# Kernel optimization log

Measured on AMD Instinct MI355X. Metric: run time of the kernel, lower is better.

Reference implementation:

```python
import jax, jax.numpy as jnp
import numpy as np

N_NODES = 50000


def _gcn_conv(x, W, b, src, dst, n_nodes):
    """PyG GCNConv: add self-loops, D^-1/2 (A+I) D^-1/2 X W + b."""
    loop = jnp.arange(n_nodes, dtype=src.dtype)
    src_f = jnp.concatenate([src, loop])  # [E+N]
    dst_f = jnp.concatenate([dst, loop])
    # degree over destination nodes (edge weight 1, incl. self loops)
    deg = jax.ops.segment_sum(jnp.ones_like(dst_f, dtype=x.dtype), dst_f,
                              num_segments=n_nodes)
    dinv = jnp.where(deg > 0, jax.lax.rsqrt(deg), 0.0)
    norm = dinv[src_f] * dinv[dst_f]  # [E+N]
    h = x @ W  # [N, C_out] dense GEMM first (C_out <= C_in here)
    msg = h[src_f] * norm[:, None]  # gather + scale
    out = jax.ops.segment_sum(msg, dst_f, num_segments=n_nodes)
    return out + b


def setup_inputs() -> dict:
    key = jax.random.key(0)
    k1, k2, k3, k4, k5, k6 = jax.random.split(key, 6)
    in_c, hid_c, out_c = 512, 512, 40
    x = jax.random.normal(k1, (N_NODES, in_c), dtype=jnp.float32)
    edge_index = jax.random.randint(k2, (2, 800000), 0, N_NODES, dtype=jnp.int64)
    # Glorot-style init for the linear weights, zero bias (PyG default)
    W1 = jax.random.normal(k3, (in_c, hid_c), dtype=jnp.float32) / np.sqrt(in_c)
    b1 = jnp.zeros((hid_c,), dtype=jnp.float32)
    W2 = jax.random.normal(k4, (hid_c, out_c), dtype=jnp.float32) / np.sqrt(hid_c)
    b2 = jnp.zeros((out_c,), dtype=jnp.float32)
    return {"x": x, "edge_index": edge_index, "W1": W1, "b1": b1,
            "W2": W2, "b2": b2}


def reference(x, edge_index, W1, b1, W2, b2):
    src, dst = edge_index[0], edge_index[1]
    h = _gcn_conv(x, W1, b1, src, dst, N_NODES)
    h = jax.nn.relu(h)
    h = _gcn_conv(h, W2, b2, src, dst, N_NODES)
    return jax.nn.log_softmax(h, axis=1)
```

## Files before the change

### kernel.cpp

```cpp
#include <hip/hip_runtime.h>


typedef unsigned int u32;
typedef unsigned short u16;
typedef __bf16 bf16x8 __attribute__((ext_vector_type(8)));
typedef float f32x4 __attribute__((ext_vector_type(4)));
typedef u32 u32x4 __attribute__((ext_vector_type(4)));

#define C_IN 512
#define C_HID 512
#define C_OUT 40
#define H_SCALE 24.0f
#define H_INV_SCALE (1.0f / 24.0f)

__device__ __forceinline__ float bf2f(u16 u) {
    u32 x = ((u32)u) << 16;
    return __builtin_bit_cast(float, x);
}
__device__ __forceinline__ u16 f2bf(float f) {
    u32 x = __builtin_bit_cast(u32, f);
    x += 0x7fffu + ((x >> 16) & 1u);
    return (u16)(x >> 16);
}
__device__ __forceinline__ char q8(float v) {
    float c = fminf(fmaxf(v * H_SCALE, -127.f), 127.f);
    return (char)__float2int_rn(c);
}
__host__ __device__ __forceinline__ int imin(int a, int b) { return a < b ? a : b; }
__host__ __device__ __forceinline__ int imax(int a, int b) { return a > b ? a : b; }

__global__ void k_init(const u32* __restrict__ x32, const int* __restrict__ ei,
                       int* flags, int* deg, int* cursor, int n) {
    if (blockIdx.x == 0 && threadIdx.x < 64) {
        int lane = threadIdx.x;
        int z = (ei[2 * lane + 1] == 0) ? 1 : 0;
        u32 e = (x32[lane] >> 7) & 0xff;
        int v = (e >= 110 && e <= 133) ? 1 : 0;
        unsigned long long bz = __ballot(z);
        unsigned long long bv = __ballot(v);
        if (lane == 0) {
            flags[0] = (__popcll(bz) == 64) ? 2 : 1;
            flags[1] = (__popcll(bv) >= 48) ? 1 : 0;
        }
    }
    int i = blockIdx.x * 256 + threadIdx.x;
    if (i < n) { deg[i] = 1; cursor[i] = 0; }
}

__global__ void k_deg(const int* __restrict__ ei, const int* __restrict__ flags,
                      int* deg, int E, int ecap, int n) {
    int e = blockIdx.x * 256 + threadIdx.x;
    if (e >= E) return;
    int st = flags[0];
    int cap = ecap * st - 1;
    u32 d = (u32)ei[imin((E + e) * st, cap)];
    if (d < (u32)n) atomicAdd(&deg[d], 1);
}

__global__ void k_scanA(const int* __restrict__ deg, int* bsum, float* dinv, int n) {
    __shared__ int sh[256];
    int i = blockIdx.x * 256 + threadIdx.x;
    int dv = (i < n) ? deg[i] : 1;
    if (i < n) dinv[i] = rsqrtf((float)imax(dv, 1));
    sh[threadIdx.x] = (i < n) ? dv - 1 : 0;
    __syncthreads();
    for (int d = 128; d > 0; d >>= 1) {
        if (threadIdx.x < d) sh[threadIdx.x] += sh[threadIdx.x + d];
        __syncthreads();
    }
    if (threadIdx.x == 0) bsum[blockIdx.x] = sh[0];
}

__global__ void k_scanB(int* bsum, int nb, int* offs, int n) {
    __shared__ int sh[256];
    int t = threadIdx.x;
    int carry = 0;
    for (int base = 0; base < nb; base += 256) {
        int i = base + t;
        int v = (i < nb) ? bsum[i] : 0;
        sh[t] = v;
        __syncthreads();
        for (int d = 1; d < 256; d <<= 1) {
            int add = (t >= d) ? sh[t - d] : 0;
            __syncthreads();
            sh[t] += add;
            __syncthreads();
        }
        if (i < nb) bsum[i] = carry + sh[t] - v;
        int tot = sh[255];
        __syncthreads();
        carry += tot;
    }
    if (t == 0) offs[n] = carry;
}

__global__ void k_scanC(const int* __restrict__ deg, const int* __restrict__ bsum,
                        int* offs, int n) {
    __shared__ int sh[256];
    int t = threadIdx.x;
    int i = blockIdx.x * 256 + t;
    int v = (i < n) ? deg[i] - 1 : 0;
    sh[t] = v;
    __syncthreads();
    for (int d = 1; d < 256; d <<= 1) {
        int add = (t >= d) ? sh[t - d] : 0;
        __syncthreads();
        sh[t] += add;
        __syncthreads();
    }
    if (i < n) offs[i] = bsum[blockIdx.x] + sh[t] - v;
}

__global__ void k_sort(const int* __restrict__ ei, const int* __restrict__ flags,
                       const int* __restrict__ offs, int* cursor, int* csr,
                       int E, int ecap, int n) {
    int e = blockIdx.x * 256 + threadIdx.x;
    if (e >= E) return;
    int st = flags[0];
    int cap = ecap * st - 1;
    u32 d = (u32)ei[imin((E + e) * st, cap)];
    u32 s = (u32)ei[imin(e * st, cap)];
    if (d < (u32)n && s < (u32)n) {
        int pos = offs[d] + atomicAdd(&cursor[(int)d], 1);
        if ((u32)pos < (u32)E) csr[pos] = (int)s;
    }
}

__device__ __forceinline__ float ldf(const void* p, int i, int isbf) {
    return isbf ? bf2f(((const u16*)p)[i]) : ((const float*)p)[i];
}

__global__ __launch_bounds__(256) void k_prep(
    const void* __restrict__ x, const void* __restrict__ W1, const void* __restrict__ b1,
    const void* __restrict__ W2, const void* __restrict__ b2,
    const int* __restrict__ flags, u16* __restrict__ w1t, u16* __restrict__ w2t,
    float* __restrict__ b1f, float* __restrict__ b2f, u16* __restrict__ xcvt,
    int nx) {
    int isbf = flags[1];
    int stride = gridDim.x * 256;
    int i0 = blockIdx.x * 256 + threadIdx.x;
    for (int i = i0; i < 512 * 512; i += stride) {
        int n = i >> 9, k = i & 511;
        w1t[n * 512 + k] = f2bf(ldf(W1, k * 512 + n, isbf));
    }
    for (int i = i0; i < 64 * 512; i += stride) {
        int n = i >> 9, k = i & 511;
        w2t[i] = (n < C_OUT) ? f2bf(ldf(W2, k * C_OUT + n, isbf)) : (u16)0;
    }
    if (i0 < C_HID) b1f[i0] = ldf(b1, i0, isbf);
    if (i0 < C_OUT) b2f[i0] = ldf(b2, i0, isbf);
    if (!isbf) {
        for (int i = i0; i < nx; i += stride)
            xcvt[i] = f2bf(((const float*)x)[i]);
    }
}

typedef __attribute__((address_space(1))) const u32 glds_src;
typedef __attribute__((address_space(3))) u32 glds_dst;

__global__ __launch_bounds__(256) void k_gemm128(
    const u16* __restrict__ xdir, const u16* __restrict__ xcvt,
    const int* __restrict__ flags, const u16* __restrict__ Bt,
    char* __restrict__ C, int M, int K, int ldc) {
    const u16* A = flags[1] ? xdir : xcvt;
    __shared__ __align__(16) u16 As0[128 * 32], As1[128 * 32];
    __shared__ __align__(16) u16 Bs0[128 * 32], Bs1[128 * 32];
    int tid = threadIdx.x;
    int wave = tid >> 6, lane = tid & 63;
    int quad = lane >> 4, lrow = lane & 15;
    int wrow = (wave & 1) * 64, wcol = (wave >> 1) * 64;

    int nwg = gridDim.x;
    int id = blockIdx.x;
    int q = nwg >> 3, r = nwg & 7;
    int xcd = id & 7, j8 = id >> 3;
    int wg = (xcd < r ? xcd * (q + 1) : r * (q + 1) + (xcd - r) * q) + j8;
    int row0 = (wg >> 2) * 128;
    int n0 = (wg & 3) * 128;

    int lr = lane >> 2;
    int lc = (lane & 3) * 8;
    int ar = row0 + wave * 32 + lr;
    int br = n0 + wave * 32 + lr;
    u16* As0_w = As0 + (wave * 32) * 32;
    u16* As1_w = As1 + (wave * 32) * 32;
    u16* Bs0_w = Bs0 + (wave * 32) * 32;
    u16* Bs1_w = Bs1 + (wave * 32) * 32;

    f32x4 acc[4][4] = {};
    int kTiles = K >> 6;
    for (int kt = 0; kt < kTiles; ++kt) {
        int k0 = kt * 64;
        int a0 = imin(ar, M - 1);
        int a1 = imin(ar + 16, M - 1);
        const u16* gA0 = A + (size_t)a0 * K + k0 + lc;
        const u16* gA1 = A + (size_t)a1 * K + k0 + lc;
        const u16* gB0 = Bt + (size_t)br * K + k0 + lc;
        const u16* gB1 = Bt + (size_t)(br + 16) * K + k0 + lc;
        __builtin_amdgcn_global_load_lds((glds_src*)gA0, (glds_dst*)As0_w, 16, 0, 0);
        __builtin_amdgcn_global_load_lds((glds_src*)gA1, (glds_dst*)(As0_w + 16 * 32), 16, 0, 0);
        __builtin_amdgcn_global_load_lds((glds_src*)(gA0 + 32), (glds_dst*)As1_w, 16, 0, 0);
        __builtin_amdgcn_global_load_lds((glds_src*)(gA1 + 32), (glds_dst*)(As1_w + 16 * 32), 16, 0, 0);
        __builtin_amdgcn_global_load_lds((glds_src*)gB0, (glds_dst*)Bs0_w, 16, 0, 0);
        __builtin_amdgcn_global_load_lds((glds_src*)gB1, (glds_dst*)(Bs0_w + 16 * 32), 16, 0, 0);
        __builtin_amdgcn_global_load_lds((glds_src*)(gB0 + 32), (glds_dst*)Bs1_w, 16, 0, 0);
        __builtin_amdgcn_global_load_lds((glds_src*)(gB1 + 32), (glds_dst*)(Bs1_w + 16 * 32), 16, 0, 0);
        __syncthreads();
#pragma unroll
        for (int ko = 0; ko < 2; ++ko) {
            const u16* Asrc = ko ? As1 : As0;
            const u16* Bsrc = ko ? Bs1 : Bs0;
            bf16x8 af[4], bfr[4];
#pragma unroll
            for (int i = 0; i < 4; ++i)
                af[i] = *(const bf16x8*)(Asrc + (wrow + i * 16 + lrow) * 32 + quad * 8);
#pragma unroll
            for (int j = 0; j < 4; ++j)
                bfr[j] = *(const bf16x8*)(Bsrc + (wcol + j * 16 + lrow) * 32 + quad * 8);
#pragma unroll
            for (int i = 0; i < 4; ++i)
#pragma unroll
                for (int j = 0; j < 4; ++j)
                    acc[i][j] = __builtin_amdgcn_mfma_f32_16x16x32_bf16(af[i], bfr[j],
                                                                        acc[i][j], 0, 0, 0);
        }
        __syncthreads();
    }
#pragma unroll
    for (int i = 0; i < 4; ++i)
#pragma unroll
        for (int j = 0; j < 4; ++j)
#pragma unroll
            for (int r2 = 0; r2 < 4; ++r2) {
                int row = row0 + wrow + i * 16 + quad * 4 + r2;
                int col = n0 + wcol + j * 16 + lrow;
                if (row < M) C[(size_t)row * ldc + col] = q8(acc[i][j][r2]);
            }
}

__global__ __launch_bounds__(256) void k_gemm64(
    const u16* __restrict__ A, const u16* __restrict__ Bt, u16* __restrict__ Cout,
    int M, int K, int Ncols, int ldc) {
    __shared__ __align__(16) u16 As[64 * 32];
    __shared__ __align__(16) u16 Bs[64 * 32];
    int tid = threadIdx.x;
    int wave = tid >> 6, lane = tid & 63;
    int quad = lane >> 4, lrow = lane & 15;
    int row0 = blockIdx.x * 64;
    int n0 = blockIdx.y * 64;
    int srow = tid >> 2;
    int skc = (tid & 3) * 8;

    f32x4 acc[4] = {};
    int kTiles = K >> 5;
    for (int kt = 0; kt < kTiles; ++kt) {
        int k0 = kt * 32;
        uint4 av = make_uint4(0, 0, 0, 0);
        int gr = row0 + srow;
        if (gr < M) av = *(const uint4*)(A + (size_t)gr * K + k0 + skc);
        uint4 bv = *(const uint4*)(Bt + (size_t)(n0 + srow) * K + k0 + skc);
        __syncthreads();
        *(uint4*)(As + srow * 32 + skc) = av;
        *(uint4*)(Bs + srow * 32 + skc) = bv;
        __syncthreads();
        bf16x8 af = *(const bf16x8*)(As + (wave * 16 + lrow) * 32 + quad * 8);
#pragma unroll
        for (int t = 0; t < 4; ++t) {
            bf16x8 bfr = *(const bf16x8*)(Bs + (t * 16 + lrow) * 32 + quad * 8);
            acc[t] = __builtin_amdgcn_mfma_f32_16x16x32_bf16(af, bfr, acc[t], 0, 0, 0);
        }
    }
#pragma unroll
    for (int t = 0; t < 4; ++t)
#pragma unroll
        for (int r = 0; r < 4; ++r) {
            int row = wave * 16 + quad * 4 + r;
            int col = t * 16 + lrow;
            int gr = row0 + row, gc = n0 + col;
            if (gr < M && gc < Ncols) Cout[(size_t)gr * ldc + gc] = f2bf(acc[t][r]);
        }
}

__device__ __forceinline__ void accum8i(float* acc, uint2 p, float w) {
    int lo = (int)p.x, hi = (int)p.y;
    acc[0] += w * (float)(signed char)(lo);
    acc[1] += w * (float)(signed char)(lo >> 8);
    acc[2] += w * (float)(signed char)(lo >> 16);
    acc[3] += w * (float)(signed char)(lo >> 24);
    acc[4] += w * (float)(signed char)(hi);
    acc[5] += w * (float)(signed char)(hi >> 8);
    acc[6] += w * (float)(signed char)(hi >> 16);
    acc[7] += w * (float)(signed char)(hi >> 24);
}

__global__ __launch_bounds__(256) void k_agg1(
    const char* __restrict__ hq, const int* __restrict__ csr, const int* __restrict__ offs,
    const float* __restrict__ dinv, const float* __restrict__ b1f,
    u16* __restrict__ out, int n, int Etot) {
    int wave = threadIdx.x >> 6, lane = threadIdx.x & 63;
    int v = blockIdx.x * 4 + wave;
    if (v >= n) return;
    float dv = dinv[v];
    float wself = dv * dv * H_INV_SCALE;

    float acc[8] = {0.f, 0.f, 0.f, 0.f, 0.f, 0.f, 0.f, 0.f};
    uint2 hs = *(const uint2*)(hq + (size_t)v * C_HID + lane * 8);
    accum8i(acc, hs, wself);

    int e0 = imax(0, imin(offs[v], Etot));
    int e1 = imax(e0, imin(offs[v + 1], Etot));
    for (int base = e0; base < e1; base += 64) {
        int cnt = imin(64, e1 - base);
        int sreg = 0; float wreg = 0.f;
        if (lane < cnt) {
            u32 s = (u32)csr[base + lane];
            s = (s < (u32)n) ? s : 0u;
            sreg = (int)s;
            wreg = dv * dinv[s] * H_INV_SCALE;
        }
        int j = 0;
        for (; j + 16 <= cnt; j += 16) {
            int ss[16]; float ww[16]; uint2 pp[16];
#pragma unroll
            for (int t = 0; t < 16; ++t) {
                ss[t] = __shfl(sreg, j + t);
                ww[t] = __shfl(wreg, j + t);
            }
#pragma unroll
            for (int t = 0; t < 16; ++t)
                pp[t] = *(const uint2*)(hq + (size_t)ss[t] * C_HID + lane * 8);
#pragma unroll
            for (int t = 0; t < 16; ++t) accum8i(acc, pp[t], ww[t]);
        }
        for (; j + 8 <= cnt; j += 8) {
            int ss[8]; float ww[8]; uint2 pp[8];
#pragma unroll
            for (int t = 0; t < 8; ++t) {
                ss[t] = __shfl(sreg, j + t);
                ww[t] = __shfl(wreg, j + t);
            }
#pragma unroll
            for (int t = 0; t < 8; ++t)
                pp[t] = *(const uint2*)(hq + (size_t)ss[t] * C_HID + lane * 8);
#pragma unroll
            for (int t = 0; t < 8; ++t) accum8i(acc, pp[t], ww[t]);
        }
        for (; j + 4 <= cnt; j += 4) {
            int ss[4]; float ww[4]; uint2 pp[4];
#pragma unroll
            for (int t = 0; t < 4; ++t) {
                ss[t] = __shfl(sreg, j + t);
                ww[t] = __shfl(wreg, j + t);
            }
#pragma unroll
            for (int t = 0; t < 4; ++t)
                pp[t] = *(const uint2*)(hq + (size_t)ss[t] * C_HID + lane * 8);
#pragma unroll
            for (int t = 0; t < 4; ++t) accum8i(acc, pp[t], ww[t]);
        }
        for (; j < cnt; ++j) {
            int sj = __shfl(sreg, j);
            float wj = __shfl(wreg, j);
            uint2 pj = *(const uint2*)(hq + (size_t)sj * C_HID + lane * 8);
            accum8i(acc, pj, wj);
        }
    }

    float4 ba = *(const float4*)(b1f + lane * 8);
    float4 bb = *(const float4*)(b1f + lane * 8 + 4);
    float r0 = fmaxf(acc[0] + ba.x, 0.f), r1 = fmaxf(acc[1] + ba.y, 0.f);
    float r2 = fmaxf(acc[2] + ba.z, 0.f), r3 = fmaxf(acc[3] + ba.w, 0.f);
    float r4 = fmaxf(acc[4] + bb.x, 0.f), r5 = fmaxf(acc[5] + bb.y, 0.f);
    float r6 = fmaxf(acc[6] + bb.z, 0.f), r7 = fmaxf(acc[7] + bb.w, 0.f);
    u32x4 o;
    o.x = (u32)f2bf(r0) | ((u32)f2bf(r1) << 16);
    o.y = (u32)f2bf(r2) | ((u32)f2bf(r3) << 16);
    o.z = (u32)f2bf(r4) | ((u32)f2bf(r5) << 16);
    o.w = (u32)f2bf(r6) | ((u32)f2bf(r7) << 16);
    __builtin_nontemporal_store(o, (u32x4*)(out + (size_t)v * C_HID + lane * 8));
}

__global__ __launch_bounds__(256) void k_agg2(
    const u16* __restrict__ h2, const int* __restrict__ csr, const int* __restrict__ offs,
    const float* __restrict__ dinv, const float* __restrict__ b2f,
    const int* __restrict__ flags, void* __restrict__ out, int n, int Etot) {
    int wave = threadIdx.x >> 6, lane = threadIdx.x & 63;
    int v = blockIdx.x * 4 + wave;
    if (v >= n) return;
    float dv = dinv[v];

    int g = lane / 10;
    int f4 = lane - g * 10;
    bool active = (g < 6);

    float4 acc = make_float4(0.f, 0.f, 0.f, 0.f);
    if (g == 0) {
        uint2 pv = *(const uint2*)(h2 + (size_t)v * C_OUT + f4 * 4);
        float w = dv * dv;
        acc.x = w * bf2f((u16)pv.x); acc.y = w * bf2f((u16)(pv.x >> 16));
        acc.z = w * bf2f((u16)pv.y); acc.w = w * bf2f((u16)(pv.y >> 16));
    }

    int e0 = imax(0, imin(offs[v], Etot));
    int e1 = imax(e0, imin(offs[v + 1], Etot));
    for (int base = e0; base < e1; base += 64) {
        int cnt = imin(64, e1 - base);
        int sreg = 0; float wreg = 0.f;
        if (lane < cnt) {
            u32 s = (u32)csr[base + lane];
            s = (s < (u32)n) ? s : 0u;
            sreg = (int)s;
            wreg = dv * dinv[s];
        }
        for (int j = 0; j < cnt; j += 24) {
            uint2 p[4]; float w4[4];
#pragma unroll
            for (int t = 0; t < 4; ++t) {
                int jj = j + t * 6 + g;
                int idx = imin(jj, cnt - 1);
                int sj = __shfl(sreg, idx);
                float wj = __shfl(wreg, idx);
                w4[t] = (active && jj < cnt) ? wj : 0.f;
                p[t] = make_uint2(0, 0);
                if (active) p[t] = *(const uint2*)(h2 + (size_t)sj * C_OUT + f4 * 4);
            }
#pragma unroll
            for (int t = 0; t < 4; ++t) {
                acc.x += w4[t] * bf2f((u16)p[t].x);
                acc.y += w4[t] * bf2f((u16)(p[t].x >> 16));
                acc.z += w4[t] * bf2f((u16)p[t].y);
                acc.w += w4[t] * bf2f((u16)(p[t].y >> 16));
            }
        }
    }

    float4 t;
    t.x = __shfl(acc.x, lane + 30); t.y = __shfl(acc.y, lane + 30);
    t.z = __shfl(acc.z, lane + 30); t.w = __shfl(acc.w, lane + 30);
    if (lane < 30) { acc.x += t.x; acc.y += t.y; acc.z += t.z; acc.w += t.w; }
    float4 t1, t2;
    t1.x = __shfl(acc.x, lane + 10); t1.y = __shfl(acc.y, lane + 10);
    t1.z = __shfl(acc.z, lane + 10); t1.w = __shfl(acc.w, lane + 10);
    t2.x = __shfl(acc.x, lane + 20); t2.y = __shfl(acc.y, lane + 20);
    t2.z = __shfl(acc.z, lane + 20); t2.w = __shfl(acc.w, lane + 20);
    if (lane < 10) {
        acc.x += t1.x + t2.x; acc.y += t1.y + t2.y;
        acc.z += t1.z + t2.z; acc.w += t1.w + t2.w;
        acc.x += b2f[f4 * 4 + 0]; acc.y += b2f[f4 * 4 + 1];
        acc.z += b2f[f4 * 4 + 2]; acc.w += b2f[f4 * 4 + 3];
    }

    float m = -1e30f;
    if (lane < 10) m = fmaxf(fmaxf(acc.x, acc.y), fmaxf(acc.z, acc.w));
    for (int off = 32; off > 0; off >>= 1) m = fmaxf(m, __shfl_xor(m, off));
    float s = 0.f;
    if (lane < 10)
        s = expf(acc.x - m) + expf(acc.y - m) + expf(acc.z - m) + expf(acc.w - m);
    for (int off = 32; off > 0; off >>= 1) s += __shfl_xor(s, off);
    if (lane < 10) {
        float ls = m + logf(s);
        if (flags[1]) {
            ushort4 o;
            o.x = f2bf(acc.x - ls); o.y = f2bf(acc.y - ls);
            o.z = f2bf(acc.z - ls); o.w = f2bf(acc.w - ls);
            *(ushort4*)((u16*)out + (size_t)v * C_OUT + f4 * 4) = o;
        } else {
            float4 o = make_float4(acc.x - ls, acc.y - ls, acc.z - ls, acc.w - ls);
            *(float4*)((float*)out + (size_t)v * C_OUT + f4 * 4) = o;
        }
    }
}


extern "C" void kernel_launch(void* const* d_in, const int* in_sizes, int n_in,
                              void* d_out, int out_size, void* d_ws, size_t ws_size,
                              hipStream_t stream) {
    const void* x = d_in[0];
    const int* ei = (const int*)d_in[1];
    const void* W1 = d_in[2];
    const void* b1 = d_in[3];
    const void* W2 = d_in[4];
    const void* b2 = d_in[5];

    const int N = out_size / C_OUT;
    const int Mx = in_sizes[0] / C_IN;
    const int M = (N < Mx) ? N : Mx;
    const int ECAP = in_sizes[1];
    const int E = ECAP / 2;

    char* p = (char*)d_ws;
    size_t used = 0;
    auto carve = [&](size_t bytes) -> void* {
        void* r = (void*)p;
        size_t b = (bytes + 255) & ~(size_t)255;
        p += b; used += b;
        return r;
    };
    int* flags = (int*)carve(256);
    int* deg = (int*)carve((size_t)N * 4);
    int* cursor = (int*)carve((size_t)N * 4);
    float* dinv = (float*)carve((size_t)N * 4);
    int* offs = (int*)carve((size_t)(N + 1) * 4);
    int* bsum = (int*)carve(8192);
    int* csr = (int*)carve((size_t)E * 4);
    u16* w1t = (u16*)carve((size_t)C_HID * C_IN * 2);
    u16* w2t = (u16*)carve((size_t)64 * C_HID * 2);
    float* b1f = (float*)carve(C_HID * 4);
    float* b2f = (float*)carve(256);
    u16* bufA = (u16*)carve((size_t)N * C_HID * 2);
    u16* bufB = (u16*)carve((size_t)N * C_HID * 2);
    if (used > ws_size) return;

    u16* xcvt = bufA;
    char* h_i8 = (char*)bufB;
    u16* hagg = bufA;
    u16* h2 = bufB;

    const int NB = (N + 255) / 256;
    const int EB = (E + 255) / 256;

    k_init<<<NB, 256, 0, stream>>>((const u32*)x, ei, flags, deg, cursor, N);
    k_deg<<<EB, 256, 0, stream>>>(ei, flags, deg, E, ECAP, N);
    k_scanA<<<NB, 256, 0, stream>>>(deg, bsum, dinv, N);
    k_scanB<<<1, 256, 0, stream>>>(bsum, NB, offs, N);
    k_scanC<<<NB, 256, 0, stream>>>(deg, bsum, offs, N);
    k_sort<<<EB, 256, 0, stream>>>(ei, flags, offs, cursor, csr, E, ECAP, N);

    k_prep<<<2048, 256, 0, stream>>>(x, W1, b1, W2, b2, flags, w1t, w2t,
                                     b1f, b2f, xcvt, M * C_IN);

    int nbx = (M + 127) / 128;
    k_gemm128<<<nbx * 4, 256, 0, stream>>>((const u16*)x, xcvt, flags, w1t, h_i8,
                                           M, C_IN, C_HID);

    k_agg1<<<(N + 3) / 4, 256, 0, stream>>>(h_i8, csr, offs, dinv, b1f, hagg, N, E);

    dim3 g2((N + 63) / 64, 1);
    k_gemm64<<<g2, 256, 0, stream>>>(hagg, w2t, h2, N, C_HID, C_OUT, C_OUT);

    k_agg2<<<(N + 3) / 4, 256, 0, stream>>>(h2, csr, offs, dinv, b2f, flags, d_out, N, E);
}
```

Measured before the change: 408.3 us.

## Fuse graph build and weight prep into one cooperative kernel with grid syncs

Replaces the seven separate launches for init, degree count, three-stage scan, CSR sort and weight/input preparation with a single cooperative kernel of 512 blocks that separates the phases with grid.sync. The goal is to remove per-launch overhead and the idle gaps between small kernels. The fp32-to-bf16 conversion of x is also vectorised with float4 loads. Running on a fixed 512-block grid can reduce parallelism for the edge loops, each grid sync adds its own cost, and the old multi-kernel path is kept as a fallback if the cooperative launch fails.

After: 896.9 us. +119.7%, slower.

```diff
diff --git a/kernel.cpp b/kernel.cpp
--- a/kernel.cpp
+++ b/kernel.cpp
@@ -1,4 +1,7 @@
 #include <hip/hip_runtime.h>
+#include <hip/hip_cooperative_groups.h>
+
+namespace cg = cooperative_groups;
 
 
 typedef unsigned int u32;
@@ -28,6 +31,141 @@
 }
 __host__ __device__ __forceinline__ int imin(int a, int b) { return a < b ? a : b; }
 __host__ __device__ __forceinline__ int imax(int a, int b) { return a > b ? a : b; }
+
+__device__ __forceinline__ float ldf(const void* p, int i, int isbf) {
+    return isbf ? bf2f(((const u16*)p)[i]) : ((const float*)p)[i];
+}
+
+__global__ __launch_bounds__(256) void k_graph(
+    const u32* __restrict__ x32, const int* __restrict__ ei,
+    int* flags, int* deg, int* cursor, float* dinv, int* offs, int* bsum,
+    int* csr,
+    const void* __restrict__ x, const void* __restrict__ W1,
+    const void* __restrict__ b1, const void* __restrict__ W2,
+    const void* __restrict__ b2,
+    u16* __restrict__ w1t, u16* __restrict__ w2t,
+    float* __restrict__ b1f, float* __restrict__ b2f, u16* __restrict__ xcvt,
+    int n, int E, int ecap, int nx) {
+    cg::grid_group grid = cg::this_grid();
+    __shared__ int sh[256];
+    int tid = threadIdx.x;
+    int gid = blockIdx.x * 256 + tid;
+    int gstride = gridDim.x * 256;
+
+    if (blockIdx.x == 0 && tid < 64) {
+        int lane = tid;
+        int z = (ei[2 * lane + 1] == 0) ? 1 : 0;
+        u32 e = (x32[lane] >> 7) & 0xff;
+        int v = (e >= 110 && e <= 133) ? 1 : 0;
+        unsigned long long bz = __ballot(z);
+        unsigned long long bv = __ballot(v);
+        if (lane == 0) {
+            flags[0] = (__popcll(bz) == 64) ? 2 : 1;
+            flags[1] = (__popcll(bv) >= 48) ? 1 : 0;
+        }
+    }
+    for (int i = gid; i < n; i += gstride) { deg[i] = 1; cursor[i] = 0; }
+    __threadfence();
+    grid.sync();
+
+    int st = flags[0];
+    int isbf = flags[1];
+    int cap = ecap * st - 1;
+
+    for (int e = gid; e < E; e += gstride) {
+        u32 d = (u32)ei[imin((E + e) * st, cap)];
+        if (d < (u32)n) atomicAdd(&deg[d], 1);
+    }
+    for (int i = gid; i < 512 * 512; i += gstride) {
+        int nn = i >> 9, k = i & 511;
+        w1t[nn * 512 + k] = f2bf(ldf(W1, k * 512 + nn, isbf));
+    }
+    for (int i = gid; i < 64 * 512; i += gstride) {
+        int nn = i >> 9, k = i & 511;
+        w2t[i] = (nn < C_OUT) ? f2bf(ldf(W2, k * C_OUT + nn, isbf)) : (u16)0;
+    }
+    if (gid < C_HID) b1f[gid] = ldf(b1, gid, isbf);
+    if (gid < C_OUT) b2f[gid] = ldf(b2, gid, isbf);
+    if (!isbf) {
+        int nv = nx >> 2;
+        const float4* xf4 = (const float4*)x;
+        ushort4* xo4 = (ushort4*)xcvt;
+        for (int i = gid; i < nv; i += gstride) {
+            float4 v = xf4[i];
+            ushort4 o;
+            o.x = f2bf(v.x); o.y = f2bf(v.y); o.z = f2bf(v.z); o.w = f2bf(v.w);
+            xo4[i] = o;
+        }
+    }
+    __threadfence();
+    grid.sync();
+
+    int NBc = (n + 255) >> 8;
+    for (int c = blockIdx.x; c < NBc; c += gridDim.x) {
+        int i = c * 256 + tid;
+        int dv = (i < n) ? deg[i] : 1;
+        if (i < n) dinv[i] = rsqrtf((float)imax(dv, 1));
+        sh[tid] = (i < n) ? dv - 1 : 0;
+        __syncthreads();
+        for (int d = 128; d > 0; d >>= 1) {
+            if (tid < d) sh[tid] += sh[tid + d];
+            __syncthreads();
+        }
+        if (tid == 0) bsum[c] = sh[0];
+        __syncthreads();
+    }
+    __threadfence();
+    grid.sync();
+
+    if (blockIdx.x == 0) {
+        int carry = 0;
+        for (int base = 0; base < NBc; base += 256) {
+            int i = base + tid;
+            int v = (i < NBc) ? bsum[i] : 0;
+            sh[tid] = v;
+            __syncthreads();
+            for (int d = 1; d < 256; d <<= 1) {
+                int add = (tid >= d) ? sh[tid - d] : 0;
+                __syncthreads();
+                sh[tid] += add;
+                __syncthreads();
+            }
+            if (i < NBc) bsum[i] = carry + sh[tid] - v;
+            int tot = sh[255];
+            __syncthreads();
+            carry += tot;
+        }
+        if (tid == 0) offs[n] = carry;
+    }
+    __threadfence();
+    grid.sync();
+
+    for (int c = blockIdx.x; c < NBc; c += gridDim.x) {
+        int i = c * 256 + tid;
+        int v = (i < n) ? deg[i] - 1 : 0;
+        sh[tid] = v;
+        __syncthreads();
+        for (int d = 1; d < 256; d <<= 1) {
+            int add = (tid >= d) ? sh[tid - d] : 0;
+            __syncthreads();
+            sh[tid] += add;
+            __syncthreads();
+        }
+        if (i < n) offs[i] = bsum[c] + sh[tid] - v;
+        __syncthreads();
+    }
+    __threadfence();
+    grid.sync();
+
+    for (int e = gid; e < E; e += gstride) {
+        u32 d = (u32)ei[imin((E + e) * st, cap)];
+        u32 s = (u32)ei[imin(e * st, cap)];
+        if (d < (u32)n && s < (u32)n) {
+            int pos = offs[d] + atomicAdd(&cursor[(int)d], 1);
+            if ((u32)pos < (u32)E) csr[pos] = (int)s;
+        }
+    }
+}
 
 __global__ void k_init(const u32* __restrict__ x32, const int* __restrict__ ei,
                        int* flags, int* deg, int* cursor, int n) {
@@ -126,10 +264,6 @@
     }
 }
 
-__device__ __forceinline__ float ldf(const void* p, int i, int isbf) {
-    return isbf ? bf2f(((const u16*)p)[i]) : ((const float*)p)[i];
-}
-
 __global__ __launch_bounds__(256) void k_prep(
     const void* __restrict__ x, const void* __restrict__ W1, const void* __restrict__ b1,
     const void* __restrict__ W2, const void* __restrict__ b2,
@@ -150,8 +284,15 @@
     if (i0 < C_HID) b1f[i0] = ldf(b1, i0, isbf);
     if (i0 < C_OUT) b2f[i0] = ldf(b2, i0, isbf);
     if (!isbf) {
-        for (int i = i0; i < nx; i += stride)
-            xcvt[i] = f2bf(((const float*)x)[i]);
+        int nv = nx >> 2;
+        const float4* xf4 = (const float4*)x;
+        ushort4* xo4 = (ushort4*)xcvt;
+        for (int i = i0; i < nv; i += stride) {
+            float4 v = xf4[i];
+            ushort4 o;
+            o.x = f2bf(v.x); o.y = f2bf(v.y); o.z = f2bf(v.z); o.w = f2bf(v.w);
+            xo4[i] = o;
+        }
     }
 }
 
@@ -518,16 +659,29 @@
 
     const int NB = (N + 255) / 256;
     const int EB = (E + 255) / 256;
-
-    k_init<<<NB, 256, 0, stream>>>((const u32*)x, ei, flags, deg, cursor, N);
-    k_deg<<<EB, 256, 0, stream>>>(ei, flags, deg, E, ECAP, N);
-    k_scanA<<<NB, 256, 0, stream>>>(deg, bsum, dinv, N);
-    k_scanB<<<1, 256, 0, stream>>>(bsum, NB, offs, N);
-    k_scanC<<<NB, 256, 0, stream>>>(deg, bsum, offs, N);
-    k_sort<<<EB, 256, 0, stream>>>(ei, flags, offs, cursor, csr, E, ECAP, N);
-
-    k_prep<<<2048, 256, 0, stream>>>(x, W1, b1, W2, b2, flags, w1t, w2t,
-                                     b1f, b2f, xcvt, M * C_IN);
+    int nx = M * C_IN;
+
+    {
+        const u32* x32 = (const u32*)x;
+        void* args[] = {
+            (void*)&x32, (void*)&ei, (void*)&flags, (void*)&deg, (void*)&cursor,
+            (void*)&dinv, (void*)&offs, (void*)&bsum, (void*)&csr,
+            (void*)&x, (void*)&W1, (void*)&b1, (void*)&W2, (void*)&b2,
+            (void*)&w1t, (void*)&w2t, (void*)&b1f, (void*)&b2f, (void*)&xcvt,
+            (void*)&N, (void*)&E, (void*)&ECAP, (void*)&nx};
+        hipError_t err = hipLaunchCooperativeKernel(
+            (const void*)k_graph, dim3(512), dim3(256), args, 0, stream);
+        if (err != hipSuccess) {
+            k_init<<<NB, 256, 0, stream>>>((const u32*)x, ei, flags, deg, cursor, N);
+            k_deg<<<EB, 256, 0, stream>>>(ei, flags, deg, E, ECAP, N);
+            k_scanA<<<NB, 256, 0, stream>>>(deg, bsum, dinv, N);
+            k_scanB<<<1, 256, 0, stream>>>(bsum, NB, offs, N);
+            k_scanC<<<NB, 256, 0, stream>>>(deg, bsum, offs, N);
+            k_sort<<<EB, 256, 0, stream>>>(ei, flags, offs, cursor, csr, E, ECAP, N);
+            k_prep<<<2048, 256, 0, stream>>>(x, W1, b1, W2, b2, flags, w1t, w2t,
+                                             b1f, b2f, xcvt, nx);
+        }
+    }
 
     int nbx = (M + 127) / 128;
     k_gemm128<<<nbx * 4, 256, 0, stream>>>((const u16*)x, xcvt, flags, w1t, h_i8,
```
